# Kernel optimization log

Hardware: AMD Instinct MI355X
Metric: run time of the kernel (lower is better)

Reference implementation:

```python
import jax, jax.numpy as jnp
import numpy as np

HIDDEN = 2048
N_HEADS = 16
HEAD_DIM = HIDDEN // N_HEADS
SEQ = 4096
ROPE_BASE = 10000.0


def setup_inputs() -> dict:
    key = jax.random.key(0)
    ks = jax.random.split(key, 5)
    sc = 1.0 / np.sqrt(HIDDEN)
    return {
        "hidden_states": jax.random.normal(ks[0], (SEQ, HIDDEN), jnp.float32),
        "Wq": jax.random.normal(ks[1], (HIDDEN, HIDDEN), jnp.float32) * sc,
        "Wk": jax.random.normal(ks[2], (HIDDEN, HIDDEN), jnp.float32) * sc,
        "Wv": jax.random.normal(ks[3], (HIDDEN, HIDDEN), jnp.float32) * sc,
        "Wo": jax.random.normal(ks[4], (HIDDEN, HIDDEN), jnp.float32) * sc,
    }


def _rope_cos_sin(seq_len, head_dim, dtype):
    # Llama-style rotary embedding tables, shape [S, 1, head_dim]
    inv_freq = 1.0 / (ROPE_BASE ** (jnp.arange(0, head_dim, 2, dtype=jnp.float32) / head_dim))
    pos = jnp.arange(seq_len, dtype=jnp.float32)
    freqs = pos[:, None] * inv_freq[None, :]          # [S, d/2]
    emb = jnp.concatenate([freqs, freqs], axis=-1)     # [S, d]
    return jnp.cos(emb)[:, None, :].astype(dtype), jnp.sin(emb)[:, None, :].astype(dtype)


def _rotate_half(x):
    h = x.shape[-1] // 2
    return jnp.concatenate([-x[..., h:], x[..., :h]], axis=-1)


def reference(hidden_states, Wq, Wk, Wv, Wo):
    S, H = hidden_states.shape
    d = HEAD_DIM
    # QKV projections (nn.Linear: x @ W.T), split into heads: [S, nH, d]
    q = (hidden_states @ Wq.T).reshape(S, N_HEADS, d)
    k = (hidden_states @ Wk.T).reshape(S, N_HEADS, d)
    v = (hidden_states @ Wv.T).reshape(S, N_HEADS, d)
    # Per-position RoPE on q and k
    cos, sin = _rope_cos_sin(S, d, q.dtype)
    q = q * cos + _rotate_half(q) * sin
    k = k * cos + _rotate_half(k) * sin
    # Causal scaled-dot-product attention, scores [nH, S, S]
    scores = jnp.einsum("snd,tnd->nst", q, k) / jnp.sqrt(jnp.asarray(d, q.dtype))
    causal = jnp.tril(jnp.ones((S, S), dtype=bool))
    scores = jnp.where(causal[None, :, :], scores, jnp.asarray(-1e30, scores.dtype))
    probs = jax.nn.softmax(scores, axis=-1)
    ctx = jnp.einsum("nst,tnd->snd", probs, v).reshape(S, H)
    return ctx @ Wo.T
```

## Files before the change

### kernel.cpp

```cpp
#include <hip/hip_runtime.h>

#define SEQ 4096
#define HIDDEN 2048
#define NHEADS 16
#define HDIM 128
#define QBLK 128
#define KVB 64

typedef float f32x4 __attribute__((ext_vector_type(4)));
typedef __bf16 bf16x8 __attribute__((ext_vector_type(8)));
typedef unsigned int u32x4 __attribute__((ext_vector_type(4)));
typedef unsigned short u16x8 __attribute__((ext_vector_type(8)));
typedef unsigned short u16;

#define SCL2 0.12751747456918851f
#define RLOG 0.2076205059304601f

__device__ __forceinline__ u16 f2bf(float f) {
  unsigned u = __float_as_uint(f);
  unsigned r = 0x7fffu + ((u >> 16) & 1u);
  return (u16)((u + r) >> 16);
}
__device__ __forceinline__ float bf2f(u16 u) {
  return __uint_as_float(((unsigned)u) << 16);
}
__device__ __forceinline__ unsigned cvtpk(float a, float b) {
  unsigned r;
  asm volatile("v_cvt_pk_bf16_f32 %0, %1, %2" : "=v"(r) : "v"(a), "v"(b));
  return r;
}

__device__ __forceinline__ void gload16(const u16* g, u16* l) {
  __builtin_amdgcn_global_load_lds(
      (const __attribute__((address_space(1))) unsigned int*)g,
      (__attribute__((address_space(3))) unsigned int*)l, 16, 0, 0);
}

__device__ __forceinline__ int cumq(int q) {
  return q < 24 ? (q - 12) * 2 : 24 + (q - 24) * 3;
}

__global__ __launch_bounds__(256) void cvt5(const float* __restrict__ X,
    const float* __restrict__ Wq, const float* __restrict__ Wk,
    const float* __restrict__ Wv, const float* __restrict__ Wo,
    u16* __restrict__ dst) {
  const size_t SH = (size_t)SEQ * HIDDEN, HH = (size_t)HIDDEN * HIDDEN;
  size_t i = ((size_t)blockIdx.x * 256 + threadIdx.x) * 8;
  const float* src; size_t off;
  if (i < SH) { src = X; off = i; }
  else if (i < SH + HH) { src = Wq; off = i - SH; }
  else if (i < SH + 2 * HH) { src = Wk; off = i - SH - HH; }
  else if (i < SH + 3 * HH) { src = Wv; off = i - SH - 2 * HH; }
  else { src = Wo; off = i - SH - 3 * HH; }
  float4 a = *reinterpret_cast<const float4*>(src + off);
  float4 b = *reinterpret_cast<const float4*>(src + off + 4);
  u16x8 o;
  o[0] = f2bf(a.x); o[1] = f2bf(a.y); o[2] = f2bf(a.z); o[3] = f2bf(a.w);
  o[4] = f2bf(b.x); o[5] = f2bf(b.y); o[6] = f2bf(b.z); o[7] = f2bf(b.w);
  *reinterpret_cast<u32x4*>(dst + i) = __builtin_bit_cast(u32x4, o);
}

__global__ __launch_bounds__(256, 3) void gemm_qkv(const u16* __restrict__ Xb,
    const u16* __restrict__ Wqb, const u16* __restrict__ Wkb,
    const u16* __restrict__ Wvb, u16* __restrict__ Qo, u16* __restrict__ Ko,
    u16* __restrict__ Vt) {
  __shared__ u16 As[2][128 * 32];
  __shared__ u16 Bs[2][128 * 32];
  const int wg = blockIdx.x;
  const int swz = (wg & 7) * 192 + (wg >> 3);
  const int z = swz >> 9;
  const int rr_ = swz & 511;
  const u16 *A, *B;
  u16* C;
  int bm, bn, cst;
  if (z == 2) {
    A = Wvb; B = Xb; C = Vt;
    bm = (rr_ & 15) << 7; bn = (rr_ >> 4) << 7; cst = SEQ;
  } else {
    A = Xb; B = z ? Wkb : Wqb; C = z ? Ko : Qo;
    bm = (rr_ & 31) << 7; bn = (rr_ >> 5) << 7; cst = HIDDEN;
  }
  const int t = threadIdx.x, lane = t & 63, wave = t >> 6;
  const int lrow = lane & 15, lk = (lane >> 4) * 8;
  const int wr = wave * 32;
  const int r0 = t >> 2, c0 = (t & 3) * 8;

  f32x4 acc[2][8] = {};

#pragma unroll
  for (int is = 0; is < 2; ++is) {
    gload16(A + (size_t)(bm + is * 64 + r0) * HIDDEN + c0, &As[0][is * 2048 + t * 8]);
    gload16(B + (size_t)(bn + is * 64 + r0) * HIDDEN + c0, &Bs[0][is * 2048 + t * 8]);
  }
  __syncthreads();

  int p = 0;
  for (int kt = 0; kt < HIDDEN; kt += 32) {
    if (kt + 32 < HIDDEN) {
#pragma unroll
      for (int is = 0; is < 2; ++is) {
        gload16(A + (size_t)(bm + is * 64 + r0) * HIDDEN + kt + 32 + c0,
                &As[p ^ 1][is * 2048 + t * 8]);
        gload16(B + (size_t)(bn + is * 64 + r0) * HIDDEN + kt + 32 + c0,
                &Bs[p ^ 1][is * 2048 + t * 8]);
      }
    }
    bf16x8 af[2], bfv[8];
#pragma unroll
    for (int m = 0; m < 2; ++m)
      af[m] = __builtin_bit_cast(bf16x8,
          *reinterpret_cast<const u32x4*>(&As[p][(wr + m * 16 + lrow) * 32 + lk]));
#pragma unroll
    for (int n = 0; n < 8; ++n)
      bfv[n] = __builtin_bit_cast(bf16x8,
          *reinterpret_cast<const u32x4*>(&Bs[p][(n * 16 + lrow) * 32 + lk]));
#pragma unroll
    for (int n = 0; n < 8; ++n)
#pragma unroll
      for (int m = 0; m < 2; ++m)
        acc[m][n] = __builtin_amdgcn_mfma_f32_16x16x32_bf16(af[m], bfv[n], acc[m][n], 0, 0, 0);
    __syncthreads();
    p ^= 1;
  }

  const int rb = (lane >> 4) * 4;
  if (z < 2) {
    const float qscale = (z == 0) ? SCL2 : 1.0f;
#pragma unroll
    for (int m = 0; m < 2; ++m)
#pragma unroll
      for (int q = 0; q < 4; ++q) {
        const int s = bm + wr + m * 16 + rb + q;
#pragma unroll
        for (int n = 0; n < 4; ++n) {
          const int ii = n * 16 + lrow;
          float inv = exp2f((float)ii * -RLOG);
          float ang = (float)s * inv;
          float sn, cs;
          __sincosf(ang, &sn, &cs);
          sn *= qscale; cs *= qscale;
          float x1 = acc[m][n][q], x2 = acc[m][n + 4][q];
          acc[m][n][q] = x1 * cs - x2 * sn;
          acc[m][n + 4][q] = x2 * cs + x1 * sn;
        }
      }
  }
#pragma unroll
  for (int m = 0; m < 2; ++m)
#pragma unroll
    for (int n = 0; n < 8; ++n)
#pragma unroll
      for (int q = 0; q < 4; ++q) {
        int col;
        if (z == 2)
          col = bn + (n >> 2) * 64 + ((n >> 1) & 1) * 32 + (lrow >> 2) * 8 +
                (n & 1) * 4 + (lrow & 3);
        else
          col = bn + n * 16 + lrow;
        C[(size_t)(bm + wr + m * 16 + rb + q) * cst + col] = f2bf(acc[m][n][q]);
      }
}

__global__ __launch_bounds__(256, 3) void gemm_out(const u16* __restrict__ A,
    const u16* __restrict__ B, float* __restrict__ C) {
  __shared__ u16 As[2][128 * 32];
  __shared__ u16 Bs[2][128 * 32];
  const int wg = blockIdx.x;
  const int swz = (wg & 7) * 64 + (wg >> 3);
  const int bm = (swz & 31) << 7;
  const int bn = (swz >> 5) << 7;
  const int t = threadIdx.x, lane = t & 63, wave = t >> 6;
  const int lrow = lane & 15, lk = (lane >> 4) * 8;
  const int wr = wave * 32;
  const int r0 = t >> 2, c0 = (t & 3) * 8;

  f32x4 acc[2][8] = {};

#pragma unroll
  for (int is = 0; is < 2; ++is) {
    gload16(A + (size_t)(bm + is * 64 + r0) * HIDDEN + c0, &As[0][is * 2048 + t * 8]);
    gload16(B + (size_t)(bn + is * 64 + r0) * HIDDEN + c0, &Bs[0][is * 2048 + t * 8]);
  }
  __syncthreads();

  int p = 0;
  for (int kt = 0; kt < HIDDEN; kt += 32) {
    if (kt + 32 < HIDDEN) {
#pragma unroll
      for (int is = 0; is < 2; ++is) {
        gload16(A + (size_t)(bm + is * 64 + r0) * HIDDEN + kt + 32 + c0,
                &As[p ^ 1][is * 2048 + t * 8]);
        gload16(B + (size_t)(bn + is * 64 + r0) * HIDDEN + kt + 32 + c0,
                &Bs[p ^ 1][is * 2048 + t * 8]);
      }
    }
    bf16x8 af[2], bfv[8];
#pragma unroll
    for (int m = 0; m < 2; ++m)
      af[m] = __builtin_bit_cast(bf16x8,
          *reinterpret_cast<const u32x4*>(&As[p][(wr + m * 16 + lrow) * 32 + lk]));
#pragma unroll
    for (int n = 0; n < 8; ++n)
      bfv[n] = __builtin_bit_cast(bf16x8,
          *reinterpret_cast<const u32x4*>(&Bs[p][(n * 16 + lrow) * 32 + lk]));
#pragma unroll
    for (int n = 0; n < 8; ++n)
#pragma unroll
      for (int m = 0; m < 2; ++m)
        acc[m][n] = __builtin_amdgcn_mfma_f32_16x16x32_bf16(af[m], bfv[n], acc[m][n], 0, 0, 0);
    __syncthreads();
    p ^= 1;
  }

  const int rb = (lane >> 4) * 4;
#pragma unroll
  for (int m = 0; m < 2; ++m)
#pragma unroll
    for (int n = 0; n < 8; ++n)
#pragma unroll
      for (int q = 0; q < 4; ++q)
        C[(size_t)(bm + wr + m * 16 + rb + q) * HIDDEN + bn + n * 16 + lrow] =
            acc[m][n][q];
}

__global__ __launch_bounds__(512, 4) void attn_kernel(const u16* __restrict__ Q,
                                                      const u16* __restrict__ Kg,
                                                      const u16* __restrict__ Vt,
                                                      u16* __restrict__ O,
                                                      u16* __restrict__ Opart,
                                                      float* __restrict__ Ml) {
  __shared__ u16 Ks[2][KVB * 128];
  __shared__ u16 Vs[2][128 * KVB];
  const int t = threadIdx.x;
  const int wave = t >> 6;
  const int lane = t & 63;
  const int lrow = lane & 15;
  const int lgrp = lane >> 4;

  const int g = blockIdx.x;
  const int h = g & 15;
  const int e = g >> 4;
  int q, c, nc;
  if (e < 24)      { q = 24 + e / 3;           c = e % 3;         nc = 3; }
  else if (e < 48) { q = 23 - ((e - 24) >> 1); c = (e - 24) & 1;  nc = 2; }
  else             { q = 59 - e;               c = 0;             nc = 1; }
  const int total = 2 * q + 2;
  const int base = total / nc, rem = total - base * nc;
  const int it0 = c * base + (c < rem ? c : rem);
  const int it1 = it0 + base + (c < rem ? 1 : 0);

  const int qw = q * QBLK + wave * 16;

  bf16x8 qf[4];
#pragma unroll
  for (int kk = 0; kk < 4; ++kk)
    qf[kk] = __builtin_bit_cast(bf16x8, *reinterpret_cast<const u32x4*>(
        Q + (size_t)(qw + lrow) * HIDDEN + h * HDIM + kk * 32 + lgrp * 8));

  const u16* kgb[2]; const u16* vgb[2]; int kof[2], vof[2];
#pragma unroll
  for (int is = 0; is < 2; ++is) {
    int ch = is * 512 + t;
    int krow = ch >> 4, kslot = ch & 15;
    int kcol = ((kslot & 8) | ((kslot ^ krow) & 7)) * 8;
    kgb[is] = Kg + (size_t)krow * HIDDEN + h * HDIM + kcol;
    kof[is] = ch * 8;
    int vrow = ch >> 3, vslot = ch & 7;
    int vcol = ((vslot ^ vrow) & 7) * 8;
    vgb[is] = Vt + (size_t)(h * HDIM + vrow) * SEQ + vcol;
    vof[is] = ch * 8;
  }

  f32x4 acc[8] = {};
  float m2 = -1e30f;
  float lsum = 0.f;

#pragma unroll
  for (int is = 0; is < 2; ++is) {
    gload16(kgb[is] + (size_t)(it0 * KVB) * HIDDEN, &Ks[0][kof[is]]);
    gload16(vgb[is] + it0 * KVB, &Vs[0][vof[is]]);
  }
  __syncthreads();

  int p = 0;
  for (int bt = it0; bt < it1; ++bt) {
    const int t0 = bt * KVB;
    if (bt + 1 < it1) {
      const int t1 = (bt + 1) * KVB;
#pragma unroll
      for (int is = 0; is < 2; ++is) {
        gload16(kgb[is] + (size_t)t1 * HIDDEN, &Ks[p ^ 1][kof[is]]);
        gload16(vgb[is] + t1, &Vs[p ^ 1][vof[is]]);
      }
    }

    if (t0 <= qw + 15) {
      const bool need_mask = (t0 + KVB - 1 > qw);
      f32x4 sc[4] = {};
      __builtin_amdgcn_s_setprio(1);
#pragma unroll
      for (int kk = 0; kk < 4; ++kk) {
#pragma unroll
        for (int colf = 0; colf < 4; ++colf) {
          int trow = colf * 16 + lrow;
          int slot = kk * 4 + lgrp;
          bf16x8 kf = __builtin_bit_cast(bf16x8, *reinterpret_cast<const u32x4*>(
              &Ks[p][trow * 128 + ((slot & 8) | ((slot ^ trow) & 7)) * 8]));
          sc[colf] = __builtin_amdgcn_mfma_f32_16x16x32_bf16(kf, qf[kk], sc[colf], 0, 0, 0);
        }
      }
      __builtin_amdgcn_s_setprio(0);

      const int qg = qw + lrow;
      float mx = -3.0e38f;
#pragma unroll
      for (int colf = 0; colf < 4; ++colf) {
        const int kvb0 = t0 + colf * 16 + lgrp * 4;
#pragma unroll
        for (int r = 0; r < 4; ++r) {
          float v = sc[colf][r];
          if (need_mask) v = (kvb0 + r <= qg) ? v : -1e30f;
          sc[colf][r] = v;
          mx = fmaxf(mx, v);
        }
      }
      mx = fmaxf(mx, __shfl_xor(mx, 16));
      mx = fmaxf(mx, __shfl_xor(mx, 32));

      if (__any(mx > m2 + 11.5f)) {
        float mn = fmaxf(m2, mx);
        float sf = exp2f(m2 - mn);
        m2 = mn;
        lsum *= sf;
#pragma unroll
        for (int r = 0; r < 4; ++r) {
          float sfr = __shfl(sf, (lane & 48) | (lgrp * 4 + r));
#pragma unroll
          for (int nn = 0; nn < 8; ++nn) acc[nn][r] *= sfr;
        }
      }

      unsigned paw[2][4];
      float ps = 0.f;
#pragma unroll
      for (int colf = 0; colf < 4; ++colf) {
        float pv[4];
#pragma unroll
        for (int r = 0; r < 4; ++r) {
          pv[r] = exp2f(sc[colf][r] - m2);
          ps += pv[r];
        }
        paw[colf >> 1][(colf & 1) * 2 + 0] = cvtpk(pv[0], pv[1]);
        paw[colf >> 1][(colf & 1) * 2 + 1] = cvtpk(pv[2], pv[3]);
      }
      ps += __shfl_xor(ps, 16);
      ps += __shfl_xor(ps, 32);
      lsum += ps;

      __builtin_amdgcn_s_setprio(1);
#pragma unroll
      for (int ks = 0; ks < 2; ++ks) {
        u32x4 w = {paw[ks][0], paw[ks][1], paw[ks][2], paw[ks][3]};
        bf16x8 pa = __builtin_bit_cast(bf16x8, w);
#pragma unroll
        for (int nn = 0; nn < 8; ++nn) {
          const int d = nn * 16 + lrow;
          bf16x8 vb = __builtin_bit_cast(bf16x8, *reinterpret_cast<const u32x4*>(
              &Vs[p][d * 64 + (((ks * 4 + lgrp) ^ d) & 7) * 8]));
          acc[nn] = __builtin_amdgcn_mfma_f32_16x16x32_bf16(pa, vb, acc[nn], 0, 0, 0);
        }
      }
      __builtin_amdgcn_s_setprio(0);
    }

    __syncthreads();
    p ^= 1;
  }

  if (nc == 1) {
    float inv[4];
#pragma unroll
    for (int r = 0; r < 4; ++r) {
      float lsr = __shfl(lsum, (lane & 48) | (lgrp * 4 + r));
      inv[r] = 1.0f / lsr;
    }
#pragma unroll
    for (int nn = 0; nn < 8; ++nn)
#pragma unroll
      for (int r = 0; r < 4; ++r) {
        int row = qw + lgrp * 4 + r;
        int col = h * HDIM + nn * 16 + lrow;
        O[(size_t)row * HIDDEN + col] = f2bf(acc[nn][r] * inv[r]);
      }
  } else {
    const int slot = h * 48 + cumq(q) + c;
    u16* Op = Opart + (size_t)slot * (QBLK * HDIM);
    float* ml = Ml + (size_t)slot * 256;
#pragma unroll
    for (int nn = 0; nn < 8; ++nn)
#pragma unroll
      for (int r = 0; r < 4; ++r) {
        int rl = wave * 16 + lgrp * 4 + r;
        Op[rl * HDIM + nn * 16 + lrow] = f2bf(acc[nn][r]);
      }
    if (lgrp == 0) {
      int rl = wave * 16 + lrow;
      ml[rl] = m2;
      ml[128 + rl] = lsum;
    }
  }
}

__global__ __launch_bounds__(256) void combine_kernel(const u16* __restrict__ Opart,
                                                      const float* __restrict__ Ml,
                                                      u16* __restrict__ O) {
  const int bid = blockIdx.x;
  const int h = bid / 20;
  const int q = 12 + bid % 20;
  const int nc = (q < 24) ? 2 : 3;
  const int sbase = h * 48 + cumq(q);
  const int r = threadIdx.x >> 1;
  const int d0 = (threadIdx.x & 1) * 64;

  float w[3], l = 0.f, M = -3.0e38f;
#pragma unroll
  for (int c = 0; c < 3; ++c)
    if (c < nc) M = fmaxf(M, Ml[(size_t)(sbase + c) * 256 + r]);
#pragma unroll
  for (int c = 0; c < 3; ++c)
    if (c < nc) {
      w[c] = exp2f(Ml[(size_t)(sbase + c) * 256 + r] - M);
      l += w[c] * Ml[(size_t)(sbase + c) * 256 + 128 + r];
    }
  const float inv = 1.0f / l;

  for (int dd = 0; dd < 64; dd += 8) {
    float a8[8] = {};
#pragma unroll
    for (int c = 0; c < 3; ++c)
      if (c < nc) {
        u16x8 v = *reinterpret_cast<const u16x8*>(
            Opart + (size_t)(sbase + c) * (QBLK * HDIM) + r * HDIM + d0 + dd);
#pragma unroll
        for (int j = 0; j < 8; ++j) a8[j] += w[c] * bf2f(v[j]);
      }
    u16x8 o8;
#pragma unroll
    for (int j = 0; j < 8; ++j) o8[j] = f2bf(a8[j] * inv);
    *reinterpret_cast<u16x8*>(
        &O[(size_t)(q * QBLK + r) * HIDDEN + h * HDIM + d0 + dd]) = o8;
  }
}

extern "C" void kernel_launch(void* const* d_in, const int* in_sizes, int n_in,
                              void* d_out, int out_size, void* d_ws, size_t ws_size,
                              hipStream_t stream) {
  const float* X  = (const float*)d_in[0];
  const float* Wq = (const float*)d_in[1];
  const float* Wk = (const float*)d_in[2];
  const float* Wv = (const float*)d_in[3];
  const float* Wo = (const float*)d_in[4];
  float* out = (float*)d_out;

  u16* ws = (u16*)d_ws;
  const size_t SH = (size_t)SEQ * HIDDEN;
  const size_t HH = (size_t)HIDDEN * HIDDEN;
  u16* Xb  = ws;
  u16* Wqb = Xb + SH;
  u16* Wkb = Wqb + HH;
  u16* Wvb = Wkb + HH;
  u16* Wob = Wvb + HH;
  u16* Qb  = Wob + HH;
  u16* Kb  = Qb + SH;
  u16* Vtb = Kb + SH;
  u16* Cb  = Vtb + SH;

  u16* Opart = ws;
  float* Ml = (float*)(ws + (size_t)768 * 16384);

  cvt5<<<(int)((SH + 4 * HH) / 2048), 256, 0, stream>>>(X, Wq, Wk, Wv, Wo, ws);

  gemm_qkv<<<1536, 256, 0, stream>>>(Xb, Wqb, Wkb, Wvb, Qb, Kb, Vtb);

  attn_kernel<<<960, 512, 0, stream>>>(Qb, Kb, Vtb, Cb, Opart, Ml);
  combine_kernel<<<320, 256, 0, stream>>>(Opart, Ml, Cb);

  gemm_out<<<512, 256, 0, stream>>>(Cb, Wob, out);
}
```

Measured before the change: 347.3 us.

## Triple-buffer QKV GEMM shared-memory tiles with partial vmcnt waits

```diff
diff --git a/kernel.cpp b/kernel.cpp
--- a/kernel.cpp
+++ b/kernel.cpp
@@ -64,8 +64,8 @@
     const u16* __restrict__ Wqb, const u16* __restrict__ Wkb,
     const u16* __restrict__ Wvb, u16* __restrict__ Qo, u16* __restrict__ Ko,
     u16* __restrict__ Vt) {
-  __shared__ u16 As[2][128 * 32];
-  __shared__ u16 Bs[2][128 * 32];
+  __shared__ u16 As[3][4096];
+  __shared__ u16 Bs[3][4096];
   const int wg = blockIdx.x;
   const int swz = (wg & 7) * 192 + (wg >> 3);
   const int z = swz >> 9;
@@ -87,41 +87,49 @@
 
   f32x4 acc[2][8] = {};
 
-#pragma unroll
-  for (int is = 0; is < 2; ++is) {
-    gload16(A + (size_t)(bm + is * 64 + r0) * HIDDEN + c0, &As[0][is * 2048 + t * 8]);
-    gload16(B + (size_t)(bn + is * 64 + r0) * HIDDEN + c0, &Bs[0][is * 2048 + t * 8]);
-  }
-  __syncthreads();
-
-  int p = 0;
-  for (int kt = 0; kt < HIDDEN; kt += 32) {
-    if (kt + 32 < HIDDEN) {
-#pragma unroll
-      for (int is = 0; is < 2; ++is) {
-        gload16(A + (size_t)(bm + is * 64 + r0) * HIDDEN + kt + 32 + c0,
-                &As[p ^ 1][is * 2048 + t * 8]);
-        gload16(B + (size_t)(bn + is * 64 + r0) * HIDDEN + kt + 32 + c0,
-                &Bs[p ^ 1][is * 2048 + t * 8]);
-      }
-    }
+  const u16* Ab = A + (size_t)(bm + r0) * HIDDEN + c0;
+  const u16* Bb = B + (size_t)(bn + r0) * HIDDEN + c0;
+  const size_t rstep = (size_t)64 * HIDDEN;
+
+#define QKV_STAGE(tt, s)                                            \
+  {                                                                 \
+    const int ko = (tt) * 32;                                       \
+    gload16(Ab + ko, &As[s][t * 8]);                                \
+    gload16(Bb + ko, &Bs[s][t * 8]);                                \
+    gload16(Ab + rstep + ko, &As[s][2048 + t * 8]);                 \
+    gload16(Bb + rstep + ko, &Bs[s][2048 + t * 8]);                 \
+  }
+
+  QKV_STAGE(0, 0);
+  QKV_STAGE(1, 1);
+  asm volatile("s_waitcnt vmcnt(4)" ::: "memory");
+  __builtin_amdgcn_s_barrier();
+  asm volatile("" ::: "memory");
+
+  int sa = 0, sb = 1, sc = 2;
+  for (int tt = 0; tt < 64; ++tt) {
+    if (tt + 2 < 64) QKV_STAGE(tt + 2, sc);
     bf16x8 af[2], bfv[8];
 #pragma unroll
     for (int m = 0; m < 2; ++m)
       af[m] = __builtin_bit_cast(bf16x8,
-          *reinterpret_cast<const u32x4*>(&As[p][(wr + m * 16 + lrow) * 32 + lk]));
+          *reinterpret_cast<const u32x4*>(&As[sa][(wr + m * 16 + lrow) * 32 + lk]));
 #pragma unroll
     for (int n = 0; n < 8; ++n)
       bfv[n] = __builtin_bit_cast(bf16x8,
-          *reinterpret_cast<const u32x4*>(&Bs[p][(n * 16 + lrow) * 32 + lk]));
+          *reinterpret_cast<const u32x4*>(&Bs[sa][(n * 16 + lrow) * 32 + lk]));
 #pragma unroll
     for (int n = 0; n < 8; ++n)
 #pragma unroll
       for (int m = 0; m < 2; ++m)
         acc[m][n] = __builtin_amdgcn_mfma_f32_16x16x32_bf16(af[m], bfv[n], acc[m][n], 0, 0, 0);
-    __syncthreads();
-    p ^= 1;
-  }
+    asm volatile("s_waitcnt vmcnt(4)" ::: "memory");
+    __builtin_amdgcn_sched_barrier(0);
+    __builtin_amdgcn_s_barrier();
+    asm volatile("" ::: "memory");
+    int s_ = sa; sa = sb; sb = sc; sc = s_;
+  }
+#undef QKV_STAGE
 
   const int rb = (lane >> 4) * 4;
   if (z < 2) {
```

Result: faster. 335.2 us (-3.5%).
